# Optimization experiments

Measured on AMD Instinct MI355X. Metric: run time of the kernel, lower is better.

## Reference

```python
import math
import jax, jax.numpy as jnp
import numpy as np

NH, D, MULT, VOCAB, NLAYER = 4, 256, 128, 256, 2
N = MULT * D // NH  # 8192
EPS = 1e-5
THETA = 2.0 ** 16


def get_freqs(n):
    q = (jnp.arange(n, dtype=jnp.float32) // 2) * 2  # quantize(t, 2)
    return 1.0 / (THETA ** (q / n)) / (2 * math.pi)


def ln(x):
    # LayerNorm over last dim, no affine
    mu = jnp.mean(x, axis=-1, keepdims=True)
    var = jnp.mean((x - mu) ** 2, axis=-1, keepdims=True)
    return (x - mu) / jnp.sqrt(var + EPS)


def rope(phases, v):
    # phases: (T, N), v: (B, nh, T, N)
    ph = (phases % 1.0) * (2 * math.pi)
    c, s = jnp.cos(ph), jnp.sin(ph)
    v_rot = jnp.stack((-v[..., 1::2], v[..., ::2]), axis=-1).reshape(v.shape)
    return v * c + v_rot * s


def setup_inputs() -> dict:
    key = jax.random.key(0)
    ks = jax.random.split(key, 6)
    std = 0.02
    return {
        "idx": jax.random.randint(ks[0], (1, 2048), 0, VOCAB),
        "embed": jax.random.normal(ks[1], (VOCAB, D), jnp.float32) * std,
        "encoder": jax.random.normal(ks[2], (NH, D, N), jnp.float32) * std,
        "encoder_v": jax.random.normal(ks[3], (NH, D, N), jnp.float32) * std,
        "decoder": jax.random.normal(ks[4], (NH * N, D), jnp.float32) * std,
        "lm_head": jax.random.normal(ks[5], (D, VOCAB), jnp.float32) * std,
    }


def reference(idx, embed, encoder, encoder_v, decoder, lm_head):
    B, T = idx.shape
    freqs = get_freqs(N)  # (N,)
    phases = jnp.arange(T, dtype=jnp.float32)[:, None] * freqs[None, :]  # (T, N)
    # strictly-lower-triangular causal mask (tril diagonal=-1)
    t = jnp.arange(T)
    mask = (t[:, None] > t[None, :]).astype(jnp.float32)  # (T, T)

    x = ln(embed[idx][:, None])  # (B, 1, T, D)
    for _ in range(NLAYER):
        x_sparse = jax.nn.relu(jnp.einsum('bltd,hdn->bhtn', x, encoder))  # (B,nh,T,N)
        QR = rope(phases, x_sparse)
        scores = jnp.einsum('bhtn,bhsn->bhts', QR, QR) * mask  # (B,nh,T,T)
        yKV = ln(jnp.einsum('bhts,blsd->bhtd', scores, x))  # (B,nh,T,D)
        y_sparse = jax.nn.relu(jnp.einsum('bhtd,hdn->bhtn', yKV, encoder_v))
        xy = x_sparse * y_sparse  # (B,nh,T,N)
        xy = xy.transpose(0, 2, 1, 3).reshape(B, 1, T, NH * N)
        yMLP = xy @ decoder  # (B,1,T,D)
        x = ln(x + ln(yMLP))
    logits = x[:, 0] @ lm_head  # (B,T,vocab)
    return logits
```

## Files before the change

kernel.cpp:

```cpp
#include <hip/hip_runtime.h>
#include <hip/hip_bf16.h>
#include <math.h>

typedef unsigned short u16;
typedef unsigned int u32;
typedef __attribute__((ext_vector_type(8))) short short8;
typedef __attribute__((ext_vector_type(4))) float f32x4;

__device__ __forceinline__ u16 f2b(float f) {
  u32 u = __builtin_bit_cast(u32, f);
  u = (u + 0x7fffu + ((u >> 16) & 1u)) >> 16;
  return (u16)u;
}
__device__ __forceinline__ float b2f(u16 s) {
  return __builtin_bit_cast(float, (u32)s << 16);
}

__device__ __forceinline__ void ld_g2l(const u16* g, u16* l) {
  __builtin_amdgcn_global_load_lds(
      (const __attribute__((address_space(1))) unsigned int*)g,
      (__attribute__((address_space(3))) unsigned int*)l, 16, 0, 0);
}

__device__ __forceinline__ void gemm_core64(
    const u16* __restrict__ A, const u16* __restrict__ B,
    int lda, int ldb, int Klen, int kb, int bm, int bn,
    u16* __restrict__ A0, u16* __restrict__ A1,
    u16* __restrict__ B0, u16* __restrict__ B1, f32x4 (&acc)[4][4])
{
  int tid = threadIdx.x;
  int w = tid >> 6, lane = tid & 63;
  int srow = (w << 4) + (lane >> 2);
  int scol = (lane & 3) << 3;
  const u16* ga0 = A + (long)(bm * 128 + srow) * lda + kb + scol;
  const u16* ga1 = ga0 + (long)64 * lda;
  const u16* gb0 = B + (long)(bn * 128 + srow) * ldb + kb + scol;
  const u16* gb1 = gb0 + (long)64 * ldb;
  int lo = w << 9;

  int wm = (w >> 1) << 6, wn = (w & 1) << 6;
  int lane15 = lane & 15, quad = lane >> 4;
  int fro = (wm + lane15) * 32 + quad * 8;
  int fco = (wn + lane15) * 32 + quad * 8;

#pragma unroll
  for (int i = 0; i < 4; i++)
#pragma unroll
    for (int j = 0; j < 4; j++) { f32x4 z = {0.f, 0.f, 0.f, 0.f}; acc[i][j] = z; }

  for (int k = 0; k < Klen; k += 64) {
    ld_g2l(ga0 + k,      A0 + lo); ld_g2l(ga1 + k,      A0 + lo + 2048);
    ld_g2l(ga0 + k + 32, A1 + lo); ld_g2l(ga1 + k + 32, A1 + lo + 2048);
    ld_g2l(gb0 + k,      B0 + lo); ld_g2l(gb1 + k,      B0 + lo + 2048);
    ld_g2l(gb0 + k + 32, B1 + lo); ld_g2l(gb1 + k + 32, B1 + lo + 2048);
    __syncthreads();
#pragma unroll
    for (int kg = 0; kg < 2; kg++) {
      const u16* ar = (kg ? A1 : A0) + fro;
      const u16* br = (kg ? B1 : B0) + fco;
      short8 af[4], bfr[4];
#pragma unroll
      for (int mt = 0; mt < 4; mt++) af[mt] = *(const short8*)(ar + mt * 512);
#pragma unroll
      for (int nt = 0; nt < 4; nt++) bfr[nt] = *(const short8*)(br + nt * 512);
#pragma unroll
      for (int mt = 0; mt < 4; mt++)
#pragma unroll
        for (int nt = 0; nt < 4; nt++)
          acc[mt][nt] = __builtin_amdgcn_mfma_f32_16x16x32_bf16(af[mt], bfr[nt], acc[mt][nt], 0, 0, 0);
    }
    __syncthreads();
  }
}

__device__ __forceinline__ void tri_decode(int t, int& bm, int& bn) {
  bm = (int)((sqrtf(8.0f * t + 1.0f) - 1.0f) * 0.5f);
  while ((bm + 1) * (bm + 2) / 2 <= t) bm++;
  while (bm * (bm + 1) / 2 > t) bm--;
  bn = t - bm * (bm + 1) / 2;
}

template<int EPI>
__global__ __launch_bounds__(256, 2) void gemm_bt(
    const u16* __restrict__ A, const u16* __restrict__ B, void* __restrict__ C,
    int K, int lda, int ldb, int ldc, int nsplits, long aB, long bB, long cB,
    int tri)
{
  __shared__ __align__(16) u16 A0[4096], A1[4096], B0[4096], B1[4096];
  int bn = blockIdx.x, bm = blockIdx.y;
  int batch = blockIdx.z / nsplits, sp = blockIdx.z % nsplits;
  int Klen = K / nsplits, kb = sp * Klen;
  if (tri) {
    int kend = (bm + 1) * 128;
    if (kb >= kend) return;
    if (kb + Klen > kend) Klen = kend - kb;
  }

  f32x4 acc[4][4];
  gemm_core64(A + (long)batch * aB, B + (long)batch * bB, lda, ldb, Klen, kb,
              bm, bn, A0, A1, B0, B1, acc);

  int lane = threadIdx.x & 63, w = threadIdx.x >> 6;
  int wm = (w >> 1) << 6, wn = (w & 1) << 6;
  int lane15 = lane & 15, quad = lane >> 4;

  if (EPI == 1 || EPI == 4) {
    u16* Cp = (u16*)C;
#pragma unroll
    for (int nt = 0; nt < 4; nt++) {
      int gn = bn * 128 + wn + nt * 16 + lane15;
      float f = exp2f((float)(-(gn & ~1)) * (1.0f / 512.0f)) * 0.15915494f;
      int t0 = bm * 128 + wm + quad * 4;
      float ph0 = (float)t0 * f; ph0 -= floorf(ph0);
      float s0, c0; __sincosf(ph0 * 6.2831853f, &s0, &c0);
      float s1, c1; __sincosf(f * 6.2831853f, &s1, &c1);
      float ph16 = 16.f * f; ph16 -= floorf(ph16);
      float s16, c16; __sincosf(ph16 * 6.2831853f, &s16, &c16);
      float cm = c0, sm = s0;
#pragma unroll
      for (int mt = 0; mt < 4; mt++) {
        float cr = cm, sr = sm;
#pragma unroll
        for (int r = 0; r < 4; r++) {
          int gm = bm * 128 + wm + mt * 16 + quad * 4 + r;
          float v = acc[mt][nt][r];
          long ci = (long)batch * cB + (long)gm * ldc + gn;
          if (EPI == 1) {
            float rv = fmaxf(v, 0.f);
            float ro = __shfl_xor(rv, 1);
            float out = (gn & 1) ? (rv * cr + ro * sr) : (rv * cr - ro * sr);
            Cp[ci] = f2b(out);
          } else {
            float qv = b2f(Cp[ci]);
            float qo = __shfl_xor(qv, 1);
            float xs = (gn & 1) ? (qv * cr - qo * sr) : (qv * cr + qo * sr);
            Cp[ci] = f2b(fmaxf(v, 0.f) * xs);
          }
          float cn = cr * c1 - sr * s1; sr = sr * c1 + cr * s1; cr = cn;
        }
        float cn2 = cm * c16 - sm * s16; sm = sm * c16 + cm * s16; cm = cn2;
      }
    }
  } else {
#pragma unroll
    for (int mt = 0; mt < 4; mt++)
#pragma unroll
      for (int nt = 0; nt < 4; nt++) {
        int gn = bn * 128 + wn + nt * 16 + lane15;
#pragma unroll
        for (int r = 0; r < 4; r++) {
          int gm = bm * 128 + wm + mt * 16 + quad * 4 + r;
          float v = acc[mt][nt][r];
          long ci = (long)batch * cB + (long)gm * ldc + gn;
          if (EPI == 0) ((float*)C)[ci] = v;
          else          atomicAdd(&((float*)C)[ci], v);
        }
      }
  }
}

__global__ __launch_bounds__(256, 2) void gemm_scores_sk(
    const u16* __restrict__ QR, u16* __restrict__ P, int T, int SK)
{
  __shared__ __align__(16) u16 A0[4096], A1[4096], B0[4096], B1[4096];
  int bm, bn; tri_decode(blockIdx.x, bm, bn);
  int h = blockIdx.y, sk = blockIdx.z;
  const u16* Q = QR + (long)h * (long)T * 8192;
  int Klen = 8192 / SK, kb = sk * Klen;

  f32x4 acc[4][4];
  gemm_core64(Q, Q, 8192, 8192, Klen, kb, bm, bn, A0, A1, B0, B1, acc);

  u16* Pb = P + ((long)sk * gridDim.y + h) * (long)T * T;
  int lane = threadIdx.x & 63, w = threadIdx.x >> 6;
  int wm = (w >> 1) << 6, wn = (w & 1) << 6;
  int lane15 = lane & 15, quad = lane >> 4;
#pragma unroll
  for (int mt = 0; mt < 4; mt++)
#pragma unroll
    for (int nt = 0; nt < 4; nt++)
#pragma unroll
      for (int r = 0; r < 4; r++) {
        int gm = bm * 128 + wm + mt * 16 + quad * 4 + r;
        int gn = bn * 128 + wn + nt * 16 + lane15;
        Pb[(long)gm * T + gn] = f2b(acc[mt][nt][r]);
      }
}

__global__ __launch_bounds__(256) void scores_cvt(
    u16* __restrict__ P, int T, int SK, int HB)
{
  int bm, bn; tri_decode(blockIdx.x, bm, bn);
  long slice = (long)HB * T * T;
  u16* base = P + (long)blockIdx.y * (long)T * T;
  for (int i = threadIdx.x; i < 2048; i += 256) {
    int r = i >> 4, c8 = (i & 15) << 3;
    int gm = bm * 128 + r, gn0 = bn * 128 + c8;
    long o = (long)gm * T + gn0;
    float s[8];
#pragma unroll
    for (int e = 0; e < 8; e++) s[e] = 0.f;
    for (int p = 0; p < SK; p++) {
      uint4 v = *(const uint4*)(base + p * slice + o);
      u32 vv[4] = {v.x, v.y, v.z, v.w};
#pragma unroll
      for (int e = 0; e < 4; e++) {
        s[2 * e]     += b2f((u16)(vv[e] & 0xffffu));
        s[2 * e + 1] += b2f((u16)(vv[e] >> 16));
      }
    }
    u32 out[4];
#pragma unroll
    for (int e = 0; e < 4; e++) {
      float e0 = (gm > gn0 + 2 * e)     ? s[2 * e]     : 0.f;
      float e1 = (gm > gn0 + 2 * e + 1) ? s[2 * e + 1] : 0.f;
      out[e] = (u32)f2b(e0) | ((u32)f2b(e1) << 16);
    }
    *(uint4*)(base + o) = make_uint4(out[0], out[1], out[2], out[3]);
  }
}

__global__ __launch_bounds__(256) void trans_f32_bf16(
    const float* __restrict__ src, u16* __restrict__ dst, int R, int C)
{
  __shared__ float tile[32][33];
  long off = (long)blockIdx.z * R * C;
  const float* s = src + off;
  u16* d = dst + off;
  int lx = threadIdx.x & 31, ly = threadIdx.x >> 5;
  int c = blockIdx.x * 32 + lx;
#pragma unroll
  for (int p = 0; p < 32; p += 8)
    tile[ly + p][lx] = s[(long)(blockIdx.y * 32 + ly + p) * C + c];
  __syncthreads();
  int rr = blockIdx.y * 32 + lx;
#pragma unroll
  for (int p = 0; p < 32; p += 8)
    d[(long)(blockIdx.x * 32 + ly + p) * R + rr] = f2b(tile[lx][ly + p]);
}

__device__ __forceinline__ float block_sum(float v, float* red) {
#pragma unroll
  for (int o = 32; o > 0; o >>= 1) v += __shfl_down(v, o, 64);
  int lane = threadIdx.x & 63, wid = threadIdx.x >> 6;
  if (lane == 0) red[wid] = v;
  __syncthreads();
  float r = red[0] + red[1] + red[2] + red[3];
  __syncthreads();
  return r;
}

__global__ __launch_bounds__(256) void embed_ln(
    const int* __restrict__ idx, const float* __restrict__ embed,
    float* __restrict__ x, u16* __restrict__ xb, u16* __restrict__ xT, int T)
{
  __shared__ float red[4];
  int t = blockIdx.x, d = threadIdx.x;
  float v = embed[(long)idx[t] * 256 + d];
  float mu = block_sum(v, red) * (1.f / 256.f);
  float c = v - mu;
  float var = block_sum(c * c, red) * (1.f / 256.f);
  float o = c * rsqrtf(var + 1e-5f);
  x[(long)t * 256 + d] = o;
  xb[(long)t * 256 + d] = f2b(o);
  xT[(long)d * T + t] = f2b(o);
}

__global__ __launch_bounds__(256) void row_ln(
    const float* __restrict__ in, u16* __restrict__ out)
{
  __shared__ float red[4];
  long row = blockIdx.x;
  int d = threadIdx.x;
  float v = in[row * 256 + d];
  float mu = block_sum(v, red) * (1.f / 256.f);
  float c = v - mu;
  float var = block_sum(c * c, red) * (1.f / 256.f);
  out[row * 256 + d] = f2b(c * rsqrtf(var + 1e-5f));
}

__global__ __launch_bounds__(256) void resid_ln(
    const float* __restrict__ yMLP, float* __restrict__ x,
    u16* __restrict__ xb, u16* __restrict__ xT, int T)
{
  __shared__ float red[4];
  int t = blockIdx.x, d = threadIdx.x;
  float y = yMLP[(long)t * 256 + d];
  float mu1 = block_sum(y, red) * (1.f / 256.f);
  float c1 = y - mu1;
  float var1 = block_sum(c1 * c1, red) * (1.f / 256.f);
  float l1 = c1 * rsqrtf(var1 + 1e-5f);
  float v = x[(long)t * 256 + d] + l1;
  float mu2 = block_sum(v, red) * (1.f / 256.f);
  float c2 = v - mu2;
  float var2 = block_sum(c2 * c2, red) * (1.f / 256.f);
  float o = c2 * rsqrtf(var2 + 1e-5f);
  x[(long)t * 256 + d] = o;
  xb[(long)t * 256 + d] = f2b(o);
  xT[(long)d * T + t] = f2b(o);
}

extern "C" void kernel_launch(void* const* d_in, const int* in_sizes, int n_in,
                              void* d_out, int out_size, void* d_ws, size_t ws_size,
                              hipStream_t stream) {
  const int*   idx       = (const int*)d_in[0];
  const float* embed     = (const float*)d_in[1];
  const float* encoder   = (const float*)d_in[2];
  const float* encoder_v = (const float*)d_in[3];
  const float* decoder   = (const float*)d_in[4];
  const float* lm_head   = (const float*)d_in[5];
  const int T = in_sizes[0];
  const int D = 256, NH = 4, Nn = 8192, V = 256;
  const int TB = T / 128, ntri = TB * (TB + 1) / 2;

  char* ws = (char*)d_ws;
  size_t off = 0;
  auto alloc = [&](size_t bytes) -> void* {
    void* p = ws + off; off += (bytes + 255) & ~(size_t)255; return p;
  };
  float* x_f32   = (float*)alloc((size_t)T * D * 4);
  float* yMLP    = (float*)alloc((size_t)T * D * 4);
  float* yKV_f32 = (float*)alloc((size_t)NH * T * D * 4);
  u16* x_b    = (u16*)alloc((size_t)T * D * 2);
  u16* xT     = (u16*)alloc((size_t)T * D * 2);
  u16* yKV_b  = (u16*)alloc((size_t)NH * T * D * 2);
  u16* lmT    = (u16*)alloc((size_t)D * V * 2);
  u16* encT   = (u16*)alloc((size_t)NH * Nn * D * 2);
  u16* encvT  = (u16*)alloc((size_t)NH * Nn * D * 2);
  u16* decT   = (u16*)alloc((size_t)D * NH * Nn * 2);
  size_t part_b = (size_t)8 * T * T * 2;
  int HB = 4;
  while (HB > 1 &&
         off + part_b + 256 + (size_t)HB * ((size_t)T * Nn * 2 + 256) > ws_size)
    HB >>= 1;
  int SK = 8 / HB;
  u16* scoresP = (u16*)alloc(part_b);
  u16* QRxy    = (u16*)alloc((size_t)HB * T * Nn * 2);
  if (off > ws_size) return;

  trans_f32_bf16<<<dim3(Nn / 32, D / 32, NH), 256, 0, stream>>>(encoder, encT, D, Nn);
  trans_f32_bf16<<<dim3(Nn / 32, D / 32, NH), 256, 0, stream>>>(encoder_v, encvT, D, Nn);
  trans_f32_bf16<<<dim3(D / 32, (NH * Nn) / 32, 1), 256, 0, stream>>>(decoder, decT, NH * Nn, D);
  trans_f32_bf16<<<dim3(V / 32, D / 32, 1), 256, 0, stream>>>(lm_head, lmT, D, V);

  embed_ln<<<T, 256, 0, stream>>>(idx, embed, x_f32, x_b, xT, T);

  for (int l = 0; l < 2; l++) {
    hipMemsetAsync(yMLP, 0, (size_t)T * D * 4, stream);
    for (int h0 = 0; h0 < NH; h0 += HB) {
      gemm_bt<1><<<dim3(Nn / 128, T / 128, HB), 256, 0, stream>>>(
          x_b, encT + (size_t)h0 * Nn * D, QRxy,
          D, D, D, Nn, 1, 0L, (long)Nn * D, (long)T * Nn, 0);
      gemm_scores_sk<<<dim3(ntri, HB, SK), 256, 0, stream>>>(QRxy, scoresP, T, SK);
      scores_cvt<<<dim3(ntri, HB), 256, 0, stream>>>(scoresP, T, SK, HB);
      hipMemsetAsync(yKV_f32, 0, (size_t)HB * T * D * 4, stream);
      gemm_bt<3><<<dim3(D / 128, T / 128, HB * 8), 256, 0, stream>>>(
          scoresP, xT, yKV_f32,
          T, T, T, D, 8, (long)T * T, 0L, (long)T * D, 1);
      row_ln<<<HB * T, 256, 0, stream>>>(yKV_f32, yKV_b);
      gemm_bt<4><<<dim3(Nn / 128, T / 128, HB), 256, 0, stream>>>(
          yKV_b, encvT + (size_t)h0 * Nn * D, QRxy,
          D, D, D, Nn, 1, (long)T * D, (long)Nn * D, (long)T * Nn, 0);
      gemm_bt<3><<<dim3(D / 128, T / 128, HB * 8), 256, 0, stream>>>(
          QRxy, decT + (size_t)h0 * Nn, yMLP,
          Nn, Nn, NH * Nn, D, 8, (long)T * Nn, (long)Nn, 0L, 0);
    }
    resid_ln<<<T, 256, 0, stream>>>(yMLP, x_f32, x_b, xT, T);
  }

  gemm_bt<0><<<dim3(V / 128, T / 128, 1), 256, 0, stream>>>(
      x_b, lmT, d_out, D, D, D, V, 1, 0L, 0L, 0L, 0);
}
```

Baseline: 1.396 ms.

## Use 128x256 tiles for encoder and scores GEMMs with 2-way split-K

Adds a 128x256 GEMM core (each wave computes 64x128) and uses it for the two encoder GEMMs with rope/product epilogues and for the causal scores GEMM. The scores GEMM now tiles the lower triangle in 128x256 blocks with a fixed 2-way split-K, so the partial buffer shrinks and the reduction kernel sums only two slices. The yKV accumulator is aliased into the second half of the partials buffer to save workspace. The larger tiles raise arithmetic intensity and cut block count, but they use more registers and LDS, which may lower occupancy, and the scores GEMM computes some extra tiles above the diagonal.

```diff
diff --git a/kernel.cpp b/kernel.cpp
--- a/kernel.cpp
+++ b/kernel.cpp
@@ -73,11 +73,66 @@
   }
 }
 
-__device__ __forceinline__ void tri_decode(int t, int& bm, int& bn) {
-  bm = (int)((sqrtf(8.0f * t + 1.0f) - 1.0f) * 0.5f);
-  while ((bm + 1) * (bm + 2) / 2 <= t) bm++;
-  while (bm * (bm + 1) / 2 > t) bm--;
-  bn = t - bm * (bm + 1) / 2;
+__device__ __forceinline__ void gemm_core256(
+    const u16* __restrict__ A, const u16* __restrict__ B,
+    int lda, int ldb, int Klen, int kb, int bm, int bn,
+    u16* __restrict__ A0, u16* __restrict__ A1,
+    u16* __restrict__ B0, u16* __restrict__ B1, f32x4 (&acc)[4][8])
+{
+  int tid = threadIdx.x;
+  int w = tid >> 6, lane = tid & 63;
+  int rsub = lane >> 2;
+  int scol = (lane & 3) << 3;
+  const u16* gaB = A + (long)(bm * 128 + (w << 5) + rsub) * lda + kb + scol;
+  const u16* gbB = B + (long)(bn * 256 + (w << 6) + rsub) * ldb + kb + scol;
+  int loA = w << 10;
+  int loB = w << 11;
+
+  int wr = w >> 1, wc = w & 1;
+  int lane15 = lane & 15, quad = lane >> 4;
+  int fra = (wr * 64 + lane15) * 32 + quad * 8;
+  int frb = (wc * 128 + lane15) * 32 + quad * 8;
+
+#pragma unroll
+  for (int i = 0; i < 4; i++)
+#pragma unroll
+    for (int j = 0; j < 8; j++) { f32x4 z = {0.f, 0.f, 0.f, 0.f}; acc[i][j] = z; }
+
+  for (int k = 0; k < Klen; k += 64) {
+#pragma unroll
+    for (int i = 0; i < 2; i++) {
+      ld_g2l(gaB + (long)(16 * i) * lda + k,      A0 + loA + (i << 9));
+      ld_g2l(gaB + (long)(16 * i) * lda + k + 32, A1 + loA + (i << 9));
+    }
+#pragma unroll
+    for (int i = 0; i < 4; i++) {
+      ld_g2l(gbB + (long)(16 * i) * ldb + k,      B0 + loB + (i << 9));
+      ld_g2l(gbB + (long)(16 * i) * ldb + k + 32, B1 + loB + (i << 9));
+    }
+    __syncthreads();
+#pragma unroll
+    for (int kg = 0; kg < 2; kg++) {
+      const u16* ar = (kg ? A1 : A0) + fra;
+      const u16* br = (kg ? B1 : B0) + frb;
+      short8 af[4], bfr[8];
+#pragma unroll
+      for (int mt = 0; mt < 4; mt++) af[mt] = *(const short8*)(ar + mt * 512);
+#pragma unroll
+      for (int nt = 0; nt < 8; nt++) bfr[nt] = *(const short8*)(br + nt * 512);
+#pragma unroll
+      for (int mt = 0; mt < 4; mt++)
+#pragma unroll
+        for (int nt = 0; nt < 8; nt++)
+          acc[mt][nt] = __builtin_amdgcn_mfma_f32_16x16x32_bf16(af[mt], bfr[nt], acc[mt][nt], 0, 0, 0);
+    }
+    __syncthreads();
+  }
+}
+
+__device__ __forceinline__ void tri2_decode(int t, int TB, int& bm, int& bn) {
+  int b = 0, rem = t;
+  while (rem >= TB - 2 * b) { rem -= TB - 2 * b; b++; }
+  bn = b; bm = 2 * b + rem;
 }
 
 template<int EPI>
@@ -103,117 +158,127 @@
   int lane = threadIdx.x & 63, w = threadIdx.x >> 6;
   int wm = (w >> 1) << 6, wn = (w & 1) << 6;
   int lane15 = lane & 15, quad = lane >> 4;
-
-  if (EPI == 1 || EPI == 4) {
-    u16* Cp = (u16*)C;
+#pragma unroll
+  for (int mt = 0; mt < 4; mt++)
 #pragma unroll
     for (int nt = 0; nt < 4; nt++) {
       int gn = bn * 128 + wn + nt * 16 + lane15;
-      float f = exp2f((float)(-(gn & ~1)) * (1.0f / 512.0f)) * 0.15915494f;
-      int t0 = bm * 128 + wm + quad * 4;
-      float ph0 = (float)t0 * f; ph0 -= floorf(ph0);
-      float s0, c0; __sincosf(ph0 * 6.2831853f, &s0, &c0);
-      float s1, c1; __sincosf(f * 6.2831853f, &s1, &c1);
-      float ph16 = 16.f * f; ph16 -= floorf(ph16);
-      float s16, c16; __sincosf(ph16 * 6.2831853f, &s16, &c16);
-      float cm = c0, sm = s0;
-#pragma unroll
-      for (int mt = 0; mt < 4; mt++) {
-        float cr = cm, sr = sm;
-#pragma unroll
-        for (int r = 0; r < 4; r++) {
-          int gm = bm * 128 + wm + mt * 16 + quad * 4 + r;
-          float v = acc[mt][nt][r];
-          long ci = (long)batch * cB + (long)gm * ldc + gn;
-          if (EPI == 1) {
-            float rv = fmaxf(v, 0.f);
-            float ro = __shfl_xor(rv, 1);
-            float out = (gn & 1) ? (rv * cr + ro * sr) : (rv * cr - ro * sr);
-            Cp[ci] = f2b(out);
-          } else {
-            float qv = b2f(Cp[ci]);
-            float qo = __shfl_xor(qv, 1);
-            float xs = (gn & 1) ? (qv * cr - qo * sr) : (qv * cr + qo * sr);
-            Cp[ci] = f2b(fmaxf(v, 0.f) * xs);
-          }
-          float cn = cr * c1 - sr * s1; sr = sr * c1 + cr * s1; cr = cn;
+#pragma unroll
+      for (int r = 0; r < 4; r++) {
+        int gm = bm * 128 + wm + mt * 16 + quad * 4 + r;
+        float v = acc[mt][nt][r];
+        long ci = (long)batch * cB + (long)gm * ldc + gn;
+        if (EPI == 0) ((float*)C)[ci] = v;
+        else          atomicAdd(&((float*)C)[ci], v);
+      }
+    }
+}
+
+template<int EPI>
+__global__ __launch_bounds__(256, 2) void gemm_bt256(
+    const u16* __restrict__ A, const u16* __restrict__ B, void* __restrict__ C,
+    int K, int lda, int ldb, int ldc, long aB, long bB, long cB)
+{
+  __shared__ __align__(16) u16 A0[4096], A1[4096], B0[8192], B1[8192];
+  int bn = blockIdx.x, bm = blockIdx.y, batch = blockIdx.z;
+
+  f32x4 acc[4][8];
+  gemm_core256(A + (long)batch * aB, B + (long)batch * bB, lda, ldb, K, 0,
+               bm, bn, A0, A1, B0, B1, acc);
+
+  int lane = threadIdx.x & 63, w = threadIdx.x >> 6;
+  int wr = w >> 1, wc = w & 1;
+  int lane15 = lane & 15, quad = lane >> 4;
+  u16* Cp = (u16*)C;
+
+#pragma unroll
+  for (int nt = 0; nt < 8; nt++) {
+    int gn = bn * 256 + wc * 128 + nt * 16 + lane15;
+    float f = exp2f((float)(-(gn & ~1)) * (1.0f / 512.0f)) * 0.15915494f;
+    int t0 = bm * 128 + wr * 64 + quad * 4;
+    float ph0 = (float)t0 * f; ph0 -= floorf(ph0);
+    float s0, c0; __sincosf(ph0 * 6.2831853f, &s0, &c0);
+    float s1, c1; __sincosf(f * 6.2831853f, &s1, &c1);
+    float ph16 = 16.f * f; ph16 -= floorf(ph16);
+    float s16, c16; __sincosf(ph16 * 6.2831853f, &s16, &c16);
+    float cm = c0, sm = s0;
+#pragma unroll
+    for (int mt = 0; mt < 4; mt++) {
+      float cr = cm, sr = sm;
+#pragma unroll
+      for (int r = 0; r < 4; r++) {
+        int gm = bm * 128 + wr * 64 + mt * 16 + quad * 4 + r;
+        float v = acc[mt][nt][r];
+        long ci = (long)batch * cB + (long)gm * ldc + gn;
+        if (EPI == 1) {
+          float rv = fmaxf(v, 0.f);
+          float ro = __shfl_xor(rv, 1);
+          float out = (gn & 1) ? (rv * cr + ro * sr) : (rv * cr - ro * sr);
+          Cp[ci] = f2b(out);
+        } else {
+          float qv = b2f(Cp[ci]);
+          float qo = __shfl_xor(qv, 1);
+          float xs = (gn & 1) ? (qv * cr - qo * sr) : (qv * cr + qo * sr);
+          Cp[ci] = f2b(fmaxf(v, 0.f) * xs);
         }
-        float cn2 = cm * c16 - sm * s16; sm = sm * c16 + cm * s16; cm = cn2;
+        float cn = cr * c1 - sr * s1; sr = sr * c1 + cr * s1; cr = cn;
       }
-    }
-  } else {
-#pragma unroll
-    for (int mt = 0; mt < 4; mt++)
-#pragma unroll
-      for (int nt = 0; nt < 4; nt++) {
-        int gn = bn * 128 + wn + nt * 16 + lane15;
-#pragma unroll
-        for (int r = 0; r < 4; r++) {
-          int gm = bm * 128 + wm + mt * 16 + quad * 4 + r;
-          float v = acc[mt][nt][r];
-          long ci = (long)batch * cB + (long)gm * ldc + gn;
-          if (EPI == 0) ((float*)C)[ci] = v;
-          else          atomicAdd(&((float*)C)[ci], v);
-        }
-      }
-  }
-}
-
-__global__ __launch_bounds__(256, 2) void gemm_scores_sk(
-    const u16* __restrict__ QR, u16* __restrict__ P, int T, int SK)
-{
-  __shared__ __align__(16) u16 A0[4096], A1[4096], B0[4096], B1[4096];
-  int bm, bn; tri_decode(blockIdx.x, bm, bn);
+      float cn2 = cm * c16 - sm * s16; sm = sm * c16 + cm * s16; cm = cn2;
+    }
+  }
+}
+
+__global__ __launch_bounds__(256, 2) void gemm_scores2(
+    const u16* __restrict__ QR, u16* __restrict__ P, int T, int HB)
+{
+  __shared__ __align__(16) u16 A0[4096], A1[4096], B0[8192], B1[8192];
+  int TB = T >> 7;
+  int bm, bn; tri2_decode(blockIdx.x, TB, bm, bn);
   int h = blockIdx.y, sk = blockIdx.z;
   const u16* Q = QR + (long)h * (long)T * 8192;
-  int Klen = 8192 / SK, kb = sk * Klen;
-
-  f32x4 acc[4][4];
-  gemm_core64(Q, Q, 8192, 8192, Klen, kb, bm, bn, A0, A1, B0, B1, acc);
-
-  u16* Pb = P + ((long)sk * gridDim.y + h) * (long)T * T;
+
+  f32x4 acc[4][8];
+  gemm_core256(Q, Q, 8192, 8192, 4096, sk * 4096, bm, bn, A0, A1, B0, B1, acc);
+
+  u16* Pb = P + ((long)sk * HB + h) * (long)T * T;
   int lane = threadIdx.x & 63, w = threadIdx.x >> 6;
-  int wm = (w >> 1) << 6, wn = (w & 1) << 6;
+  int wr = w >> 1, wc = w & 1;
   int lane15 = lane & 15, quad = lane >> 4;
 #pragma unroll
   for (int mt = 0; mt < 4; mt++)
 #pragma unroll
-    for (int nt = 0; nt < 4; nt++)
+    for (int nt = 0; nt < 8; nt++) {
+      int gn = bn * 256 + wc * 128 + nt * 16 + lane15;
 #pragma unroll
       for (int r = 0; r < 4; r++) {
-        int gm = bm * 128 + wm + mt * 16 + quad * 4 + r;
-        int gn = bn * 128 + wn + nt * 16 + lane15;
+        int gm = bm * 128 + wr * 64 + mt * 16 + quad * 4 + r;
         Pb[(long)gm * T + gn] = f2b(acc[mt][nt][r]);
       }
-}
-
-__global__ __launch_bounds__(256) void scores_cvt(
-    u16* __restrict__ P, int T, int SK, int HB)
-{
-  int bm, bn; tri_decode(blockIdx.x, bm, bn);
+    }
+}
+
+__global__ __launch_bounds__(256) void scores_cvt2(
+    u16* __restrict__ P, int T, int HB)
+{
+  int TB = T >> 7;
+  int bm, bn; tri2_decode(blockIdx.x, TB, bm, bn);
   long slice = (long)HB * T * T;
   u16* base = P + (long)blockIdx.y * (long)T * T;
-  for (int i = threadIdx.x; i < 2048; i += 256) {
-    int r = i >> 4, c8 = (i & 15) << 3;
-    int gm = bm * 128 + r, gn0 = bn * 128 + c8;
+  for (int i = threadIdx.x; i < 4096; i += 256) {
+    int r = i >> 5, c8 = (i & 31) << 3;
+    int gm = bm * 128 + r, gn0 = bn * 256 + c8;
     long o = (long)gm * T + gn0;
-    float s[8];
-#pragma unroll
-    for (int e = 0; e < 8; e++) s[e] = 0.f;
-    for (int p = 0; p < SK; p++) {
-      uint4 v = *(const uint4*)(base + p * slice + o);
-      u32 vv[4] = {v.x, v.y, v.z, v.w};
-#pragma unroll
-      for (int e = 0; e < 4; e++) {
-        s[2 * e]     += b2f((u16)(vv[e] & 0xffffu));
-        s[2 * e + 1] += b2f((u16)(vv[e] >> 16));
-      }
-    }
+    uint4 v0 = *(const uint4*)(base + o);
+    uint4 v1 = *(const uint4*)(base + slice + o);
+    u32 a[4] = {v0.x, v0.y, v0.z, v0.w};
+    u32 b[4] = {v1.x, v1.y, v1.z, v1.w};
     u32 out[4];
 #pragma unroll
     for (int e = 0; e < 4; e++) {
-      float e0 = (gm > gn0 + 2 * e)     ? s[2 * e]     : 0.f;
-      float e1 = (gm > gn0 + 2 * e + 1) ? s[2 * e + 1] : 0.f;
+      float e0 = b2f((u16)(a[e] & 0xffffu)) + b2f((u16)(b[e] & 0xffffu));
+      float e1 = b2f((u16)(a[e] >> 16))     + b2f((u16)(b[e] >> 16));
+      e0 = (gm > gn0 + 2 * e)     ? e0 : 0.f;
+      e1 = (gm > gn0 + 2 * e + 1) ? e1 : 0.f;
       out[e] = (u32)f2b(e0) | ((u32)f2b(e1) << 16);
     }
     *(uint4*)(base + o) = make_uint4(out[0], out[1], out[2], out[3]);
@@ -311,16 +376,17 @@
   const float* lm_head   = (const float*)d_in[5];
   const int T = in_sizes[0];
   const int D = 256, NH = 4, Nn = 8192, V = 256;
-  const int TB = T / 128, ntri = TB * (TB + 1) / 2;
+  const int TB = T / 128;
+  int ntri2 = 0;
+  for (int b = 0; b < TB / 2; b++) ntri2 += TB - 2 * b;
 
   char* ws = (char*)d_ws;
   size_t off = 0;
   auto alloc = [&](size_t bytes) -> void* {
     void* p = ws + off; off += (bytes + 255) & ~(size_t)255; return p;
   };
-  float* x_f32   = (float*)alloc((size_t)T * D * 4);
-  float* yMLP    = (float*)alloc((size_t)T * D * 4);
-  float* yKV_f32 = (float*)alloc((size_t)NH * T * D * 4);
+  float* x_f32 = (float*)alloc((size_t)T * D * 4);
+  float* yMLP  = (float*)alloc((size_t)T * D * 4);
   u16* x_b    = (u16*)alloc((size_t)T * D * 2);
   u16* xT     = (u16*)alloc((size_t)T * D * 2);
   u16* yKV_b  = (u16*)alloc((size_t)NH * T * D * 2);
@@ -328,15 +394,14 @@
   u16* encT   = (u16*)alloc((size_t)NH * Nn * D * 2);
   u16* encvT  = (u16*)alloc((size_t)NH * Nn * D * 2);
   u16* decT   = (u16*)alloc((size_t)D * NH * Nn * 2);
-  size_t part_b = (size_t)8 * T * T * 2;
   int HB = 4;
   while (HB > 1 &&
-         off + part_b + 256 + (size_t)HB * ((size_t)T * Nn * 2 + 256) > ws_size)
+         off + (size_t)HB * (2 * (size_t)T * T * 2 + (size_t)T * Nn * 2) + 512 > ws_size)
     HB >>= 1;
-  int SK = 8 / HB;
-  u16* scoresP = (u16*)alloc(part_b);
+  u16* scoresP = (u16*)alloc((size_t)2 * HB * T * T * 2);
   u16* QRxy    = (u16*)alloc((size_t)HB * T * Nn * 2);
   if (off > ws_size) return;
+  float* yKV_f32 = (float*)(scoresP + (size_t)HB * T * T);
 
   trans_f32_bf16<<<dim3(Nn / 32, D / 32, NH), 256, 0, stream>>>(encoder, encT, D, Nn);
   trans_f32_bf16<<<dim3(Nn / 32, D / 32, NH), 256, 0, stream>>>(encoder_v, encvT, D, Nn);
@@ -348,19 +413,19 @@
   for (int l = 0; l < 2; l++) {
     hipMemsetAsync(yMLP, 0, (size_t)T * D * 4, stream);
     for (int h0 = 0; h0 < NH; h0 += HB) {
-      gemm_bt<1><<<dim3(Nn / 128, T / 128, HB), 256, 0, stream>>>(
+      gemm_bt256<1><<<dim3(Nn / 256, T / 128, HB), 256, 0, stream>>>(
           x_b, encT + (size_t)h0 * Nn * D, QRxy,
-          D, D, D, Nn, 1, 0L, (long)Nn * D, (long)T * Nn, 0);
-      gemm_scores_sk<<<dim3(ntri, HB, SK), 256, 0, stream>>>(QRxy, scoresP, T, SK);
-      scores_cvt<<<dim3(ntri, HB), 256, 0, stream>>>(scoresP, T, SK, HB);
+          D, D, D, Nn, 0L, (long)Nn * D, (long)T * Nn);
+      gemm_scores2<<<dim3(ntri2, HB, 2), 256, 0, stream>>>(QRxy, scoresP, T, HB);
+      scores_cvt2<<<dim3(ntri2, HB), 256, 0, stream>>>(scoresP, T, HB);
       hipMemsetAsync(yKV_f32, 0, (size_t)HB * T * D * 4, stream);
       gemm_bt<3><<<dim3(D / 128, T / 128, HB * 8), 256, 0, stream>>>(
           scoresP, xT, yKV_f32,
           T, T, T, D, 8, (long)T * T, 0L, (long)T * D, 1);
       row_ln<<<HB * T, 256, 0, stream>>>(yKV_f32, yKV_b);
-      gemm_bt<4><<<dim3(Nn / 128, T / 128, HB), 256, 0, stream>>>(
+      gemm_bt256<4><<<dim3(Nn / 256, T / 128, HB), 256, 0, stream>>>(
           yKV_b, encvT + (size_t)h0 * Nn * D, QRxy,
-          D, D, D, Nn, 1, (long)T * D, (long)Nn * D, (long)T * Nn, 0);
+          D, D, D, Nn, (long)T * D, (long)Nn * D, (long)T * Nn);
       gemm_bt<3><<<dim3(D / 128, T / 128, HB * 8), 256, 0, stream>>>(
           QRxy, decT + (size_t)h0 * Nn, yMLP,
           Nn, Nn, NH * Nn, D, 8, (long)T * Nn, (long)Nn, 0L, 0);
```

Result: no change. 1.408 ms (+0.8%).
